# Kernel optimization log

Hardware: AMD Instinct MI355X
Metric: run time of the kernel (lower is better)

Reference implementation:

```python
import jax, jax.numpy as jnp
import numpy as np
import math

D_MODEL = 1024
D_HEAD = 64
BATCH = 8
SEQ = 2048


def setup_inputs() -> dict:
    key = jax.random.key(0)
    ks = jax.random.split(key, 5)
    s = 0.02
    return {
        "residual_stream": jax.random.normal(ks[0], (BATCH, SEQ, D_MODEL), dtype=jnp.float32),
        "Wq": jax.random.normal(ks[1], (D_HEAD, D_MODEL), dtype=jnp.float32) * s,
        "Wk": jax.random.normal(ks[2], (D_HEAD, D_MODEL), dtype=jnp.float32) * s,
        "Wv": jax.random.normal(ks[3], (D_HEAD, D_MODEL), dtype=jnp.float32) * s,
        "Wo": jax.random.normal(ks[4], (D_MODEL, D_HEAD), dtype=jnp.float32) * s,
    }


def reference(residual_stream, Wq, Wk, Wv, Wo):
    # NOTE: module scales by 1/sqrt(d_model), NOT 1/sqrt(d_head)
    scale = 1.0 / math.sqrt(D_MODEL)
    q = jnp.einsum('bsd,hd->bsh', residual_stream, Wq)  # [B,S,Dh]
    k = jnp.einsum('bsd,hd->bsh', residual_stream, Wk)  # [B,S,Dh]
    scores = jnp.einsum('bqh,bkh->bqk', q, k) * scale   # [B,S,S]
    seq = scores.shape[-1]
    causal = jnp.tril(jnp.ones((seq, seq), dtype=bool))
    scores = jnp.where(causal[None, :, :], scores, jnp.float32(-jnp.inf))
    attn = jax.nn.softmax(scores, axis=-1)
    # O applied to V *before* the attention-weighted sum (as in the module)
    x = jnp.einsum('bsh,dh->bsd', jnp.einsum('bsd,hd->bsh', residual_stream, Wv), Wo)  # [B,S,Dm]
    return jnp.einsum('bqk,bkd->bqd', attn, x)
```

## Files before the change

### kernel.cpp

```cpp
#include <hip/hip_runtime.h>

#define SEQ 2048
#define DMODEL 1024
#define DHEAD 64
#define NROWS 16384
#define ATT_SC2 0.0450842300667f

typedef __attribute__((ext_vector_type(8))) short bf16x8;
typedef __attribute__((ext_vector_type(4))) float f32x4;
typedef __attribute__((ext_vector_type(4))) unsigned int u32x4;
typedef __attribute__((ext_vector_type(4))) unsigned short u16x4;
typedef __attribute__((ext_vector_type(4))) float fl4;

#define MFMA16(a,b,c) __builtin_amdgcn_mfma_f32_16x16x32_bf16((a),(b),(c),0,0,0)
#define GLL16(g, l) __builtin_amdgcn_global_load_lds( \
    (const __attribute__((address_space(1))) void*)(g), \
    (__attribute__((address_space(3))) void*)(l), 16, 0, 0)

__device__ __forceinline__ unsigned short f2bf(float f) {
    union { float f; unsigned int u; } v; v.f = f;
    unsigned int u = v.u;
    unsigned int r = u + 0x7fffu + ((u >> 16) & 1u);
    return (unsigned short)(r >> 16);
}

__device__ __forceinline__ unsigned int cvtpk(float lo, float hi) {
    unsigned int d;
    asm volatile("v_cvt_pk_bf16_f32 %0, %1, %2" : "=v"(d) : "v"(lo), "v"(hi));
    return d;
}

__global__ __launch_bounds__(256) void k_cvt(
    const float* __restrict__ Wq, const float* __restrict__ Wk,
    const float* __restrict__ Wv, const float* __restrict__ Wo,
    unsigned short* __restrict__ Wb,
    unsigned short* __restrict__ Wob)
{
    int i4 = blockIdx.x * 256 + threadIdx.x;
    const int W1 = 16384;
    const float* src; unsigned short* dst; int off;
    if (i4 < 3 * W1) {
        int which = i4 / W1;
        off = i4 - which * W1;
        src = (which == 0) ? Wq : (which == 1) ? Wk : Wv;
        dst = Wb + (size_t)which * 65536;
    } else {
        off = i4 - 3 * W1; src = Wo; dst = Wob;
    }
    fl4 v = reinterpret_cast<const fl4*>(src)[off];
    u16x4 o;
    o[0] = f2bf(v[0]); o[1] = f2bf(v[1]); o[2] = f2bf(v[2]); o[3] = f2bf(v[3]);
    reinterpret_cast<u16x4*>(dst)[off] = o;
}

__global__ __launch_bounds__(256) void k_qkv(
    const float* __restrict__ x,
    const unsigned short* __restrict__ Wb,
    unsigned short* __restrict__ Qb,
    unsigned short* __restrict__ Kb,
    unsigned short* __restrict__ Vt)
{
    __shared__ __align__(16) char smem[81920];

    int tid = threadIdx.x;
    int wave = tid >> 6, lane = tid & 63, g = lane >> 4, lr = lane & 15;
    int mbase = blockIdx.x * 64;

    const float* xsrc[4];
#pragma unroll
    for (int j = 0; j < 4; ++j) {
        int ci = (wave * 4 + j) * 64 + lane;
        int row = ci >> 4, c = ci & 15, cg = c ^ (row & 7);
        xsrc[j] = x + (size_t)(mbase + row) * DMODEL + cg * 4;
    }
    const unsigned short* wsrc[6];
#pragma unroll
    for (int j = 0; j < 6; ++j) {
        int ci = (wave * 6 + j) * 64 + lane;
        int row = ci >> 3, c = ci & 7, cg = c ^ (row & 7);
        wsrc[j] = Wb + (size_t)row * DMODEL + cg * 8;
    }

    f32x4 acc[12];
#pragma unroll
    for (int f = 0; f < 12; ++f) acc[f] = (f32x4){0.f, 0.f, 0.f, 0.f};

#pragma unroll
    for (int j = 0; j < 4; ++j) GLL16(xsrc[j], smem + (wave * 4 + j) * 1024);
#pragma unroll
    for (int j = 0; j < 6; ++j) GLL16(wsrc[j], smem + 32768 + (wave * 6 + j) * 1024);

    for (int ks = 0; ks < 16; ++ks) {
        int cur = ks & 1;
        if (ks < 15) {
            int nb = cur ^ 1;
#pragma unroll
            for (int j = 0; j < 4; ++j)
                GLL16(xsrc[j] + (ks + 1) * 64, smem + nb * 16384 + (wave * 4 + j) * 1024);
#pragma unroll
            for (int j = 0; j < 6; ++j)
                GLL16(wsrc[j] + (ks + 1) * 64, smem + 32768 + nb * 24576 + (wave * 6 + j) * 1024);
            asm volatile("s_waitcnt vmcnt(10)" ::: "memory");
        } else {
            asm volatile("s_waitcnt vmcnt(0)" ::: "memory");
        }
        __builtin_amdgcn_s_barrier();
        asm volatile("" ::: "memory");

        const float* Xf = (const float*)(smem + cur * 16384);
        const unsigned short* Wf = (const unsigned short*)(smem + 32768 + cur * 24576);
        int arow = wave * 16 + lr;
#pragma unroll
        for (int kc = 0; kc < 2; ++kc) {
            int c0 = (kc * 8 + g * 2) ^ (lr & 7);
            int c1 = (kc * 8 + g * 2 + 1) ^ (lr & 7);
            fl4 xa = *(const fl4*)&Xf[arow * 64 + c0 * 4];
            fl4 xb = *(const fl4*)&Xf[arow * 64 + c1 * 4];
            union { unsigned int u[4]; bf16x8 v; } a;
            a.u[0] = cvtpk(xa[0], xa[1]); a.u[1] = cvtpk(xa[2], xa[3]);
            a.u[2] = cvtpk(xb[0], xb[1]); a.u[3] = cvtpk(xb[2], xb[3]);
            __builtin_amdgcn_s_setprio(1);
#pragma unroll
            for (int f = 0; f < 12; ++f) {
                int brow = f * 16 + lr;
                int cb = (kc * 4 + g) ^ (lr & 7);
                bf16x8 b = *(const bf16x8*)&Wf[brow * 64 + cb * 8];
                acc[f] = MFMA16(a.v, b, acc[f]);
            }
            __builtin_amdgcn_s_setprio(0);
        }
        asm volatile("" ::: "memory");
        __builtin_amdgcn_s_barrier();
    }

    int mrow = mbase + wave * 16 + g * 4;
#pragma unroll
    for (int f = 0; f < 8; ++f) {
        int col = f * 16 + lr;
#pragma unroll
        for (int r = 0; r < 4; ++r) {
            unsigned short bv = f2bf(acc[f][r]);
            if (f < 4) Qb[(size_t)(mrow + r) * DHEAD + col] = bv;
            else       Kb[(size_t)(mrow + r) * DHEAD + col - 64] = bv;
        }
    }
    unsigned short* tmp = (unsigned short*)smem;
#pragma unroll
    for (int f = 8; f < 12; ++f) {
        int h = (f - 8) * 16 + lr;
#pragma unroll
        for (int r = 0; r < 4; ++r)
            tmp[(wave * 16 + g * 4 + r) * 72 + h] = f2bf(acc[f][r]);
    }
    __syncthreads();
    int b = mbase >> 11, sbase = mbase & 2047;
    int h = tid >> 2, sc = tid & 3;
    u32x4 o0, o1;
#pragma unroll
    for (int j = 0; j < 4; ++j) {
        o0[j] = (unsigned int)tmp[(sc * 16 + 2 * j) * 72 + h] |
                ((unsigned int)tmp[(sc * 16 + 2 * j + 1) * 72 + h] << 16);
        o1[j] = (unsigned int)tmp[(sc * 16 + 8 + 2 * j) * 72 + h] |
                ((unsigned int)tmp[(sc * 16 + 9 + 2 * j) * 72 + h] << 16);
    }
    size_t off = ((size_t)(b * 64 + h)) * SEQ + sbase + sc * 16;
    *reinterpret_cast<u32x4*>(&Vt[off]) = o0;
    *reinterpret_cast<u32x4*>(&Vt[off + 8]) = o1;
}

__global__ __launch_bounds__(256) void k_fused(
    const unsigned short* __restrict__ Qb,
    const unsigned short* __restrict__ Kb,
    const unsigned short* __restrict__ Vt,
    const unsigned short* __restrict__ Wob,
    float* __restrict__ out)
{
    __shared__ __align__(16) char smem[73728];

    int tid = threadIdx.x;
    int wave = tid >> 6, lane = tid & 63, g = lane >> 4, lr = lane & 15;
    int pair = wave >> 1, pw = wave & 1;
    int bid = blockIdx.x;
    int idx = bid & 255;
    int qt = (bid < 256) ? (63 - (idx >> 3)) : (idx >> 3);
    int b = idx & 7;

    const unsigned short* ksrc[2];
    const unsigned short* vsrc[2];
#pragma unroll
    for (int j = 0; j < 2; ++j) {
        int ci = j * 256 + tid;
        int row = ci >> 3, c = ci & 7, cg = c ^ (row & 7);
        ksrc[j] = Kb + ((size_t)(b * SEQ) + row) * DHEAD + cg * 8;
        vsrc[j] = Vt + ((size_t)(b * DHEAD) + row) * SEQ + cg * 8;
    }

#define STAGE(n_, s_) do {                                                   \
    int te_ = (2 * (s_)) * 64;                                               \
    int to_ = ((2 * (s_) + 1 < (n_)) ? (2 * (s_) + 1) : ((n_) - 1)) * 64;    \
    char* base_ = smem + ((s_) & 1) * 32768;                                 \
    _Pragma("unroll")                                                        \
    for (int j_ = 0; j_ < 2; ++j_) {                                         \
        GLL16(ksrc[j_] + (size_t)te_ * DHEAD, base_ + j_ * 4096 + wave * 1024);          \
        GLL16(ksrc[j_] + (size_t)to_ * DHEAD, base_ + 8192 + j_ * 4096 + wave * 1024);   \
        GLL16(vsrc[j_] + te_, base_ + 16384 + j_ * 4096 + wave * 1024);                  \
        GLL16(vsrc[j_] + to_, base_ + 24576 + j_ * 4096 + wave * 1024);                  \
    } } while (0)

    int n = (qt >> 1) + 1;
    int nsteps = (n + 1) >> 1;
    int qw = qt * 32 + pw * 16;
    size_t qrowbase = (size_t)(b * SEQ) + qw;

    bf16x8 aq[2];
#pragma unroll
    for (int kc = 0; kc < 2; ++kc)
        aq[kc] = *(const bf16x8*)&Qb[(qrowbase + lr) * DHEAD + kc * 32 + g * 8];

    STAGE(n, 0);

    float l_part[4];
    f32x4 of[4];
#pragma unroll
    for (int r = 0; r < 4; ++r) l_part[r] = 0.f;
#pragma unroll
    for (int f = 0; f < 4; ++f) of[f] = (f32x4){0.f, 0.f, 0.f, 0.f};

    for (int s = 0; s < nsteps; ++s) {
        if (s + 1 < nsteps) {
            STAGE(n, s + 1);
            asm volatile("s_waitcnt vmcnt(8)" ::: "memory");
        } else {
            asm volatile("s_waitcnt vmcnt(0)" ::: "memory");
        }
        __builtin_amdgcn_s_barrier();
        asm volatile("" ::: "memory");

        int t = 2 * s + pair, kvb = t * 64;
        if (t < n && kvb <= qw + 15) {
            const unsigned short* Kl =
                (const unsigned short*)(smem + (s & 1) * 32768 + pair * 8192);
            const unsigned short* Vl =
                (const unsigned short*)(smem + (s & 1) * 32768 + 16384 + pair * 8192);
            unsigned short* Pl = (unsigned short*)(smem + 65536) + wave * 1024;

            f32x4 s4[4];
#pragma unroll
            for (int f = 0; f < 4; ++f) s4[f] = (f32x4){0.f, 0.f, 0.f, 0.f};
            __builtin_amdgcn_s_setprio(1);
#pragma unroll
            for (int kc = 0; kc < 2; ++kc) {
#pragma unroll
                for (int f = 0; f < 4; ++f) {
                    int brow = f * 16 + lr;
                    int cb = (kc * 4 + g) ^ (lr & 7);
                    bf16x8 bk = *(const bf16x8*)&Kl[brow * 64 + cb * 8];
                    s4[f] = MFMA16(aq[kc], bk, s4[f]);
                }
            }
            __builtin_amdgcn_s_setprio(0);

            if (kvb + 63 <= qw) {
#pragma unroll
                for (int f = 0; f < 4; ++f)
#pragma unroll
                    for (int r = 0; r < 4; ++r) {
                        float p = exp2f(s4[f][r] * ATT_SC2);
                        s4[f][r] = p;
                        l_part[r] += p;
                    }
            } else {
#pragma unroll
                for (int f = 0; f < 4; ++f) {
                    int kvg = kvb + f * 16 + lr;
#pragma unroll
                    for (int r = 0; r < 4; ++r) {
                        int qr = qw + g * 4 + r;
                        float p = exp2f(s4[f][r] * ATT_SC2);
                        p = (kvg > qr) ? 0.f : p;
                        s4[f][r] = p;
                        l_part[r] += p;
                    }
                }
            }
#pragma unroll
            for (int f = 0; f < 4; ++f) {
#pragma unroll
                for (int r = 0; r < 4; ++r) {
                    int row = g * 4 + r, col = f * 16 + lr;
                    int ch = (col >> 3) ^ (row & 7);
                    Pl[row * 64 + ch * 8 + (col & 7)] = f2bf(s4[f][r]);
                }
            }
#pragma unroll
            for (int kc = 0; kc < 2; ++kc) {
                int cp = (kc * 4 + g) ^ (lr & 7);
                bf16x8 ap = *(const bf16x8*)&Pl[lr * 64 + cp * 8];
                __builtin_amdgcn_s_setprio(1);
#pragma unroll
                for (int fd = 0; fd < 4; ++fd) {
                    int vrow = fd * 16 + lr;
                    int cv = (kc * 4 + g) ^ (lr & 7);
                    bf16x8 bv = *(const bf16x8*)&Vl[vrow * 64 + cv * 8];
                    of[fd] = MFMA16(ap, bv, of[fd]);
                }
                __builtin_amdgcn_s_setprio(0);
            }
        }
        asm volatile("" ::: "memory");
        __builtin_amdgcn_s_barrier();
    }

    {
        float* Obuf = (float*)(smem + pair * 8704);
        float* Ol = (float*)(smem + 17408);
        int row32 = pw * 16 + g * 4;
#pragma unroll
        for (int r = 0; r < 4; ++r) {
            float ls = l_part[r];
            ls += __shfl_xor(ls, 1); ls += __shfl_xor(ls, 2);
            ls += __shfl_xor(ls, 4); ls += __shfl_xor(ls, 8);
            if (lr == 0) Ol[pair * 32 + row32 + r] = ls;
#pragma unroll
            for (int fd = 0; fd < 4; ++fd)
                Obuf[(row32 + r) * 68 + fd * 16 + lr] = of[fd][r];
        }
    }
    __syncthreads();

    bf16x8 ao[2][2];
    {
        const float* O0 = (const float*)smem;
        const float* O1 = (const float*)(smem + 8704);
        const float* Ol = (const float*)(smem + 17408);
#pragma unroll
        for (int m = 0; m < 2; ++m) {
            int arow = m * 16 + lr;
            float inv = 1.f / (Ol[arow] + Ol[32 + arow]);
#pragma unroll
            for (int kc = 0; kc < 2; ++kc) {
                int cb = arow * 68 + kc * 32 + g * 8;
                fl4 xa = *(const fl4*)&O0[cb], xb = *(const fl4*)&O0[cb + 4];
                fl4 ya = *(const fl4*)&O1[cb], yb = *(const fl4*)&O1[cb + 4];
                union { unsigned int u[4]; bf16x8 v; } a;
                a.u[0] = cvtpk((xa[0] + ya[0]) * inv, (xa[1] + ya[1]) * inv);
                a.u[1] = cvtpk((xa[2] + ya[2]) * inv, (xa[3] + ya[3]) * inv);
                a.u[2] = cvtpk((xb[0] + yb[0]) * inv, (xb[1] + yb[1]) * inv);
                a.u[3] = cvtpk((xb[2] + yb[2]) * inv, (xb[3] + yb[3]) * inv);
                ao[m][kc] = a.v;
            }
        }
    }

    {
        int nb = wave * 256;
        f32x4 acc[2][16];
#pragma unroll
        for (int m = 0; m < 2; ++m)
#pragma unroll
            for (int f = 0; f < 16; ++f) acc[m][f] = (f32x4){0.f, 0.f, 0.f, 0.f};
#pragma unroll
        for (int kc = 0; kc < 2; ++kc) {
            __builtin_amdgcn_s_setprio(1);
#pragma unroll
            for (int f = 0; f < 16; ++f) {
                bf16x8 bw = *(const bf16x8*)
                    &Wob[(size_t)(nb + f * 16 + lr) * DHEAD + kc * 32 + g * 8];
                acc[0][f] = MFMA16(ao[0][kc], bw, acc[0][f]);
                acc[1][f] = MFMA16(ao[1][kc], bw, acc[1][f]);
            }
            __builtin_amdgcn_s_setprio(0);
        }
        int mb = b * SEQ + qt * 32;
#pragma unroll
        for (int m = 0; m < 2; ++m) {
            int mrow = mb + m * 16 + g * 4;
#pragma unroll
            for (int f = 0; f < 16; ++f)
#pragma unroll
                for (int r = 0; r < 4; ++r)
                    out[(size_t)(mrow + r) * DMODEL + nb + f * 16 + lr] = acc[m][f][r];
        }
    }
#undef STAGE
}

extern "C" void kernel_launch(void* const* d_in, const int* in_sizes, int n_in,
                              void* d_out, int out_size, void* d_ws, size_t ws_size,
                              hipStream_t stream) {
    const float* x  = (const float*)d_in[0];
    const float* Wq = (const float*)d_in[1];
    const float* Wk = (const float*)d_in[2];
    const float* Wv = (const float*)d_in[3];
    const float* Wo = (const float*)d_in[4];
    float* out = (float*)d_out;

    unsigned short* Wb  = (unsigned short*)d_ws;
    unsigned short* Wob = Wb + 196608;
    unsigned short* Qb  = Wob + 65536;
    unsigned short* Kb  = Qb + 1048576;
    unsigned short* Vt  = Kb + 1048576;

    k_cvt<<<256, 256, 0, stream>>>(Wq, Wk, Wv, Wo, Wb, Wob);
    k_qkv<<<256, 256, 0, stream>>>(x, Wb, Qb, Kb, Vt);
    k_fused<<<512, 256, 0, stream>>>(Qb, Kb, Vt, Wob, out);
}
```

Baseline: 58.06 us.

## Split QKV projection across more blocks and keep P in registers via permlane swaps

```diff
diff --git a/kernel.cpp b/kernel.cpp
--- a/kernel.cpp
+++ b/kernel.cpp
@@ -60,16 +60,17 @@
     unsigned short* __restrict__ Kb,
     unsigned short* __restrict__ Vt)
 {
-    __shared__ __align__(16) char smem[81920];
+    __shared__ __align__(16) char smem[65536];
 
     int tid = threadIdx.x;
     int wave = tid >> 6, lane = tid & 63, g = lane >> 4, lr = lane & 15;
-    int mbase = blockIdx.x * 64;
-
-    const float* xsrc[4];
-#pragma unroll
-    for (int j = 0; j < 4; ++j) {
-        int ci = (wave * 4 + j) * 64 + lane;
+    int mh = wave & 1, nh = wave >> 1;
+    int mbase = blockIdx.x * 32;
+
+    const float* xsrc[2];
+#pragma unroll
+    for (int j = 0; j < 2; ++j) {
+        int ci = j * 256 + tid;
         int row = ci >> 4, c = ci & 15, cg = c ^ (row & 7);
         xsrc[j] = x + (size_t)(mbase + row) * DMODEL + cg * 4;
     }
@@ -81,35 +82,36 @@
         wsrc[j] = Wb + (size_t)row * DMODEL + cg * 8;
     }
 
-    f32x4 acc[12];
-#pragma unroll
-    for (int f = 0; f < 12; ++f) acc[f] = (f32x4){0.f, 0.f, 0.f, 0.f};
-
-#pragma unroll
-    for (int j = 0; j < 4; ++j) GLL16(xsrc[j], smem + (wave * 4 + j) * 1024);
-#pragma unroll
-    for (int j = 0; j < 6; ++j) GLL16(wsrc[j], smem + 32768 + (wave * 6 + j) * 1024);
+    f32x4 acc[6];
+#pragma unroll
+    for (int f = 0; f < 6; ++f) acc[f] = (f32x4){0.f, 0.f, 0.f, 0.f};
+
+#pragma unroll
+    for (int j = 0; j < 2; ++j) GLL16(xsrc[j], smem + j * 4096 + wave * 1024);
+#pragma unroll
+    for (int j = 0; j < 6; ++j) GLL16(wsrc[j], smem + 16384 + (wave * 6 + j) * 1024);
 
     for (int ks = 0; ks < 16; ++ks) {
         int cur = ks & 1;
         if (ks < 15) {
             int nb = cur ^ 1;
 #pragma unroll
-            for (int j = 0; j < 4; ++j)
-                GLL16(xsrc[j] + (ks + 1) * 64, smem + nb * 16384 + (wave * 4 + j) * 1024);
+            for (int j = 0; j < 2; ++j)
+                GLL16(xsrc[j] + (ks + 1) * 64, smem + nb * 8192 + j * 4096 + wave * 1024);
 #pragma unroll
             for (int j = 0; j < 6; ++j)
-                GLL16(wsrc[j] + (ks + 1) * 64, smem + 32768 + nb * 24576 + (wave * 6 + j) * 1024);
-            asm volatile("s_waitcnt vmcnt(10)" ::: "memory");
+                GLL16(wsrc[j] + (ks + 1) * 64,
+                      smem + 16384 + nb * 24576 + (wave * 6 + j) * 1024);
+            asm volatile("s_waitcnt vmcnt(8)" ::: "memory");
         } else {
             asm volatile("s_waitcnt vmcnt(0)" ::: "memory");
         }
         __builtin_amdgcn_s_barrier();
         asm volatile("" ::: "memory");
 
-        const float* Xf = (const float*)(smem + cur * 16384);
-        const unsigned short* Wf = (const unsigned short*)(smem + 32768 + cur * 24576);
-        int arow = wave * 16 + lr;
+        const float* Xf = (const float*)(smem + cur * 8192);
+        const unsigned short* Wf = (const unsigned short*)(smem + 16384 + cur * 24576);
+        int arow = mh * 16 + lr;
 #pragma unroll
         for (int kc = 0; kc < 2; ++kc) {
             int c0 = (kc * 8 + g * 2) ^ (lr & 7);
@@ -121,8 +123,8 @@
             a.u[2] = cvtpk(xb[0], xb[1]); a.u[3] = cvtpk(xb[2], xb[3]);
             __builtin_amdgcn_s_setprio(1);
 #pragma unroll
-            for (int f = 0; f < 12; ++f) {
-                int brow = f * 16 + lr;
+            for (int f = 0; f < 6; ++f) {
+                int brow = (nh * 6 + f) * 16 + lr;
                 int cb = (kc * 4 + g) ^ (lr & 7);
                 bf16x8 b = *(const bf16x8*)&Wf[brow * 64 + cb * 8];
                 acc[f] = MFMA16(a.v, b, acc[f]);
@@ -133,39 +135,30 @@
         __builtin_amdgcn_s_barrier();
     }
 
-    int mrow = mbase + wave * 16 + g * 4;
-#pragma unroll
-    for (int f = 0; f < 8; ++f) {
-        int col = f * 16 + lr;
+    unsigned short* tmp = (unsigned short*)smem;
+    int mrow = mbase + mh * 16 + g * 4;
+#pragma unroll
+    for (int f = 0; f < 6; ++f) {
+        int fg = nh * 6 + f;
 #pragma unroll
         for (int r = 0; r < 4; ++r) {
             unsigned short bv = f2bf(acc[f][r]);
-            if (f < 4) Qb[(size_t)(mrow + r) * DHEAD + col] = bv;
-            else       Kb[(size_t)(mrow + r) * DHEAD + col - 64] = bv;
-        }
-    }
-    unsigned short* tmp = (unsigned short*)smem;
-#pragma unroll
-    for (int f = 8; f < 12; ++f) {
-        int h = (f - 8) * 16 + lr;
-#pragma unroll
-        for (int r = 0; r < 4; ++r)
-            tmp[(wave * 16 + g * 4 + r) * 72 + h] = f2bf(acc[f][r]);
+            if (fg < 4)      Qb[(size_t)(mrow + r) * DHEAD + fg * 16 + lr] = bv;
+            else if (fg < 8) Kb[(size_t)(mrow + r) * DHEAD + (fg - 4) * 16 + lr] = bv;
+            else             tmp[(mh * 16 + g * 4 + r) * 72 + (fg - 8) * 16 + lr] = bv;
+        }
     }
     __syncthreads();
     int b = mbase >> 11, sbase = mbase & 2047;
     int h = tid >> 2, sc = tid & 3;
-    u32x4 o0, o1;
+    u32x4 o;
 #pragma unroll
     for (int j = 0; j < 4; ++j) {
-        o0[j] = (unsigned int)tmp[(sc * 16 + 2 * j) * 72 + h] |
-                ((unsigned int)tmp[(sc * 16 + 2 * j + 1) * 72 + h] << 16);
-        o1[j] = (unsigned int)tmp[(sc * 16 + 8 + 2 * j) * 72 + h] |
-                ((unsigned int)tmp[(sc * 16 + 9 + 2 * j) * 72 + h] << 16);
-    }
-    size_t off = ((size_t)(b * 64 + h)) * SEQ + sbase + sc * 16;
-    *reinterpret_cast<u32x4*>(&Vt[off]) = o0;
-    *reinterpret_cast<u32x4*>(&Vt[off + 8]) = o1;
+        o[j] = (unsigned int)tmp[(sc * 8 + 2 * j) * 72 + h] |
+               ((unsigned int)tmp[(sc * 8 + 2 * j + 1) * 72 + h] << 16);
+    }
+    size_t off = ((size_t)(b * 64 + h)) * SEQ + sbase + sc * 8;
+    *reinterpret_cast<u32x4*>(&Vt[off]) = o;
 }
 
 __global__ __launch_bounds__(256) void k_fused(
@@ -175,7 +168,7 @@
     const unsigned short* __restrict__ Wob,
     float* __restrict__ out)
 {
-    __shared__ __align__(16) char smem[73728];
+    __shared__ __align__(16) char smem[65536];
 
     int tid = threadIdx.x;
     int wave = tid >> 6, lane = tid & 63, g = lane >> 4, lr = lane & 15;
@@ -219,10 +212,8 @@
 
     STAGE(n, 0);
 
-    float l_part[4];
+    float l_part = 0.f;
     f32x4 of[4];
-#pragma unroll
-    for (int r = 0; r < 4; ++r) l_part[r] = 0.f;
 #pragma unroll
     for (int f = 0; f < 4; ++f) of[f] = (f32x4){0.f, 0.f, 0.f, 0.f};
 
@@ -242,7 +233,6 @@
                 (const unsigned short*)(smem + (s & 1) * 32768 + pair * 8192);
             const unsigned short* Vl =
                 (const unsigned short*)(smem + (s & 1) * 32768 + 16384 + pair * 8192);
-            unsigned short* Pl = (unsigned short*)(smem + 65536) + wave * 1024;
 
             f32x4 s4[4];
 #pragma unroll
@@ -255,7 +245,7 @@
                     int brow = f * 16 + lr;
                     int cb = (kc * 4 + g) ^ (lr & 7);
                     bf16x8 bk = *(const bf16x8*)&Kl[brow * 64 + cb * 8];
-                    s4[f] = MFMA16(aq[kc], bk, s4[f]);
+                    s4[f] = MFMA16(bk, aq[kc], s4[f]);
                 }
             }
             __builtin_amdgcn_s_setprio(0);
@@ -267,42 +257,45 @@
                     for (int r = 0; r < 4; ++r) {
                         float p = exp2f(s4[f][r] * ATT_SC2);
                         s4[f][r] = p;
-                        l_part[r] += p;
+                        l_part += p;
                     }
             } else {
+                int qr = qw + lr;
 #pragma unroll
                 for (int f = 0; f < 4; ++f) {
-                    int kvg = kvb + f * 16 + lr;
 #pragma unroll
                     for (int r = 0; r < 4; ++r) {
-                        int qr = qw + g * 4 + r;
+                        int kvg = kvb + f * 16 + g * 4 + r;
                         float p = exp2f(s4[f][r] * ATT_SC2);
                         p = (kvg > qr) ? 0.f : p;
                         s4[f][r] = p;
-                        l_part[r] += p;
+                        l_part += p;
                     }
                 }
             }
+            unsigned int pk[4][2];
 #pragma unroll
             for (int f = 0; f < 4; ++f) {
-#pragma unroll
-                for (int r = 0; r < 4; ++r) {
-                    int row = g * 4 + r, col = f * 16 + lr;
-                    int ch = (col >> 3) ^ (row & 7);
-                    Pl[row * 64 + ch * 8 + (col & 7)] = f2bf(s4[f][r]);
-                }
+                pk[f][0] = cvtpk(s4[f][0], s4[f][1]);
+                pk[f][1] = cvtpk(s4[f][2], s4[f][3]);
             }
 #pragma unroll
             for (int kc = 0; kc < 2; ++kc) {
-                int cp = (kc * 4 + g) ^ (lr & 7);
-                bf16x8 ap = *(const bf16x8*)&Pl[lr * 64 + cp * 8];
+                unsigned int A = pk[2 * kc][0],     Bv = pk[2 * kc][1];
+                unsigned int C = pk[2 * kc + 1][0], D  = pk[2 * kc + 1][1];
+                asm("v_permlane32_swap_b32 %0, %1" : "+v"(A), "+v"(C));
+                asm("v_permlane16_swap_b32 %0, %1" : "+v"(A), "+v"(C));
+                asm("v_permlane32_swap_b32 %0, %1" : "+v"(Bv), "+v"(D));
+                asm("v_permlane16_swap_b32 %0, %1" : "+v"(Bv), "+v"(D));
+                union { unsigned int u[4]; bf16x8 v; } ap;
+                ap.u[0] = A; ap.u[1] = Bv; ap.u[2] = C; ap.u[3] = D;
                 __builtin_amdgcn_s_setprio(1);
 #pragma unroll
                 for (int fd = 0; fd < 4; ++fd) {
                     int vrow = fd * 16 + lr;
                     int cv = (kc * 4 + g) ^ (lr & 7);
                     bf16x8 bv = *(const bf16x8*)&Vl[vrow * 64 + cv * 8];
-                    of[fd] = MFMA16(ap, bv, of[fd]);
+                    of[fd] = MFMA16(ap.v, bv, of[fd]);
                 }
                 __builtin_amdgcn_s_setprio(0);
             }
@@ -314,17 +307,16 @@
     {
         float* Obuf = (float*)(smem + pair * 8704);
         float* Ol = (float*)(smem + 17408);
+        float ls = l_part;
+        ls += __shfl_xor(ls, 16);
+        ls += __shfl_xor(ls, 32);
+        if (lane < 16) Ol[pair * 32 + pw * 16 + lane] = ls;
         int row32 = pw * 16 + g * 4;
 #pragma unroll
-        for (int r = 0; r < 4; ++r) {
-            float ls = l_part[r];
-            ls += __shfl_xor(ls, 1); ls += __shfl_xor(ls, 2);
-            ls += __shfl_xor(ls, 4); ls += __shfl_xor(ls, 8);
-            if (lr == 0) Ol[pair * 32 + row32 + r] = ls;
+        for (int r = 0; r < 4; ++r)
 #pragma unroll
             for (int fd = 0; fd < 4; ++fd)
                 Obuf[(row32 + r) * 68 + fd * 16 + lr] = of[fd][r];
-        }
     }
     __syncthreads();
 
@@ -402,6 +394,6 @@
     unsigned short* Vt  = Kb + 1048576;
 
     k_cvt<<<256, 256, 0, stream>>>(Wq, Wk, Wv, Wo, Wb, Wob);
-    k_qkv<<<256, 256, 0, stream>>>(x, Wb, Qb, Kb, Vt);
+    k_qkv<<<512, 256, 0, stream>>>(x, Wb, Qb, Kb, Vt);
     k_fused<<<512, 256, 0, stream>>>(Qb, Kb, Vt, Wob, out);
 }
```

After: 55.40 us. 4.6% less time.
